# Kernel tuning notes

Hardware: AMD Instinct MI355X
Metric: run time of the kernel (lower is better)

The kernel has to match this reference:

```python
import jax, jax.numpy as jnp
import numpy as np

B, N, D, E, H = 16, 1024, 1024, 4, 16


def setup_inputs() -> dict:
    key = jax.random.key(0)
    k1, k2, k3, k4 = jax.random.split(key, 4)
    return {
        "input_tokens": jax.random.normal(k1, (B, N, D), dtype=jnp.float32),
        "expert_mask": jax.random.randint(k2, (B, N), 0, E, dtype=jnp.int32),
        "qkv_w": jax.random.normal(k3, (3 * D, D), dtype=jnp.float32) * 0.02,
        "proj_w": jax.random.normal(k4, (D, D), dtype=jnp.float32) * 0.02,
        "proj_b": jnp.zeros((D,), dtype=jnp.float32),
    }


def reference(input_tokens, expert_mask, qkv_w, proj_w, proj_b):
    b, n, d = input_tokens.shape
    hd = d // H
    scale = 1.0 / np.sqrt(hd).astype(np.float32)
    # nested expert e uses first d_e = D / 2^(E-1-e) features (expert E-1 = full dim)
    d_tok = d // (2 ** (E - 1 - expert_mask))                     # [B, N]
    feat_mask = (jnp.arange(d)[None, None, :] < d_tok[..., None]).astype(input_tokens.dtype)  # [B, N, D]
    # NestedLinearExpand: slice input features per token (== mask), full 3D output
    x_in = input_tokens * feat_mask
    qkv = jnp.einsum('bnd,fd->bnf', x_in, qkv_w).reshape(b, n, 3, H, hd)
    q, k, v = jnp.moveaxis(qkv, 2, 0)                             # each [B, N, H, hd]
    q = q.transpose(0, 2, 1, 3)                                   # [B, H, N, hd]
    k = k.transpose(0, 2, 1, 3)
    v = v.transpose(0, 2, 1, 3)
    scores = jnp.einsum('bhqd,bhkd->bhqk', q, k) * scale          # [B, H, N, N]
    attn = jax.nn.softmax(scores, axis=-1)
    x = jnp.einsum('bhqk,bhkd->bhqd', attn, v)                    # [B, H, N, hd]
    x = x.transpose(0, 2, 1, 3).reshape(b, n, d)
    # NestedLinearContract: full-dim matmul, only first d_e outputs kept per token
    y = jnp.einsum('bnd,fd->bnf', x, proj_w) + proj_b
    return y * feat_mask
```

## Files before the change

### kernel.cpp

```cpp
#include <hip/hip_runtime.h>
#include <hip/hip_bf16.h>


typedef __bf16 bf16_t;
typedef __bf16 bf16x8 __attribute__((ext_vector_type(8)));
typedef __bf16 bf16x4 __attribute__((ext_vector_type(4)));
typedef float f32x4 __attribute__((ext_vector_type(4)));
typedef float f32x16 __attribute__((ext_vector_type(16)));
typedef int i32x4 __attribute__((ext_vector_type(4)));

typedef __attribute__((address_space(1))) void gvoid;
typedef __attribute__((address_space(3))) void lvoid;

#define MFMA16(a, b, c) __builtin_amdgcn_mfma_f32_16x16x32_bf16((a), (b), (c), 0, 0, 0)
#define MFMA32(a, b, c) __builtin_amdgcn_mfma_f32_32x32x16_bf16((a), (b), (c), 0, 0, 0)
#define GLOAD_LDS16(gsrc, ldst) \
  __builtin_amdgcn_global_load_lds((gvoid*)(gsrc), (lvoid*)(ldst), 16, 0, 0)

#define QSCALE 0.18033688f

__device__ __forceinline__ unsigned cvtpk(float lo, float hi) {
  unsigned r;
  asm("v_cvt_pk_bf16_f32 %0, %1, %2" : "=v"(r) : "v"(lo), "v"(hi));
  return r;
}
__device__ __forceinline__ void pl32swap(unsigned& x, unsigned& y) {
  asm("v_permlane32_swap_b32 %0, %1" : "+v"(x), "+v"(y));
}

__global__ __launch_bounds__(256) void sort_batch(
    const int* __restrict__ em, int* __restrict__ perm, int* __restrict__ ems) {
  __shared__ int cnt[4], base[4], cur[4];
  const int b = blockIdx.x, t = threadIdx.x;
  if (t < 4) cnt[t] = 0;
  __syncthreads();
  int e[4];
#pragma unroll
  for (int i = 0; i < 4; ++i) {
    e[i] = em[b * 1024 + t * 4 + i];
    atomicAdd(&cnt[e[i]], 1);
  }
  __syncthreads();
  if (t == 0) {
    base[0] = 0; base[1] = cnt[0];
    base[2] = cnt[0] + cnt[1]; base[3] = cnt[0] + cnt[1] + cnt[2];
    cur[0] = cur[1] = cur[2] = cur[3] = 0;
  }
  __syncthreads();
#pragma unroll
  for (int i = 0; i < 4; ++i) {
    const int pos = base[e[i]] + atomicAdd(&cur[e[i]], 1);
    perm[b * 1024 + pos] = t * 4 + i;
    ems[b * 1024 + pos] = e[i];
  }
}

__global__ __launch_bounds__(256) void prep_tokens(
    const float* __restrict__ x, const int* __restrict__ perm,
    const int* __restrict__ ems, bf16_t* __restrict__ xq) {
  const int prow = blockIdx.x;
  const int orig = (prow & ~1023) + perm[prow];
  const int dt = 128 << ems[prow];
  const int d = threadIdx.x * 4;
  float4 v = ((const float4*)(x + (size_t)orig * 1024))[threadIdx.x];
  const bool keep = d < dt;
  bf16x4 o;
  o[0] = (bf16_t)(keep ? v.x : 0.f);
  o[1] = (bf16_t)(keep ? v.y : 0.f);
  o[2] = (bf16_t)(keep ? v.z : 0.f);
  o[3] = (bf16_t)(keep ? v.w : 0.f);
  *((bf16x4*)(xq + (size_t)prow * 1024 + d)) = o;
}

__global__ __launch_bounds__(256) void conv_w(
    const float* __restrict__ s, bf16_t* __restrict__ dvec) {
  const int i = blockIdx.x * 256 + threadIdx.x;
  float4 v = ((const float4*)s)[i];
  bf16x4 o;
  o[0] = (bf16_t)v.x; o[1] = (bf16_t)v.y; o[2] = (bf16_t)v.z; o[3] = (bf16_t)v.w;
  ((bf16x4*)dvec)[i] = o;
}

template <int EPI>
__global__ __launch_bounds__(512, 2) void gemm256(
    const bf16_t* __restrict__ A, const bf16_t* __restrict__ Bw, int K,
    const int* __restrict__ perm, const int* __restrict__ ems,
    bf16_t* __restrict__ qo, bf16_t* __restrict__ ko, bf16_t* __restrict__ vto,
    float* __restrict__ yout, const float* __restrict__ bias) {
  __shared__ bf16_t lds[2][32768];
  const int tid = threadIdx.x;
  const int lane = tid & 63, w = tid >> 6;
  const int wm = w >> 2, wn = w & 3;
  const int g = lane >> 4, c16 = lane & 15;

  const int bid = blockIdx.x;
  const int rowbase = (bid & 63) * 256;
  const int colbase = (bid >> 6) * 256;

  const int dtmax = 128 << ems[rowbase + 255];

  if constexpr (EPI == 1) {
    if (colbase >= dtmax) {
      const float4 z = make_float4(0.f, 0.f, 0.f, 0.f);
#pragma unroll
      for (int i = 0; i < 32; ++i) {
        const int idx = i * 512 + tid;
        const int r = idx >> 6, c4 = idx & 63;
        const int orow = ((rowbase + r) & ~1023) + perm[rowbase + r];
        ((float4*)(yout + (size_t)orow * 1024 + colbase))[c4] = z;
      }
      return;
    }
  }

  const int NT = (EPI == 0) ? (dtmax >> 6) : (K >> 6);

  const int trow = tid >> 3;
  const int scol = (((tid & 7) ^ (trow & 7)) << 3);
  const bf16_t* pa = A + (size_t)(rowbase + trow) * K + scol;
  const bf16_t* pb = Bw + (size_t)(colbase + trow) * K + scol;

#define STAGE(j, koff, dst)                                       \
  GLOAD_LDS16(((j) < 4 ? pa + (size_t)((j) * 64) * K              \
                       : pb + (size_t)(((j) - 4) * 64) * K) +     \
                  (koff),                                         \
              (dst) + ((j) * 512 + tid) * 8)

#define LDFRAG(base, R, kk)            \
  (*(const bf16x8*)((base) + (size_t)(R) * 64 + \
                    (((((kk) << 2) + g) ^ (c16 & 7)) << 3)))

  f32x4 acc[8][4] = {};

#pragma unroll
  for (int j = 0; j < 8; ++j) STAGE(j, 0, (bf16_t*)lds[0]);
  asm volatile("s_waitcnt vmcnt(0)" ::: "memory");
  __builtin_amdgcn_s_barrier();

  for (int t = 0; t < NT; ++t) {
    const bf16_t* Lb = lds[t & 1];
    const bf16_t* LbB = Lb + 16384;
    const bool pf = (t + 1) < NT;

    if (pf) {
      bf16_t* Sd = (bf16_t*)lds[(t + 1) & 1];
      const int koff = (t + 1) << 6;
#pragma unroll
      for (int j = 0; j < 8; ++j) STAGE(j, koff, Sd);
    }

    bf16x8 af[4][2], af2[4][2], b0[2][2], b1[2][2];
#pragma unroll
    for (int mi = 0; mi < 4; ++mi)
#pragma unroll
      for (int kk = 0; kk < 2; ++kk)
        af[mi][kk] = LDFRAG(Lb, wm * 128 + mi * 16 + c16, kk);
#pragma unroll
    for (int ni = 0; ni < 2; ++ni)
#pragma unroll
      for (int kk = 0; kk < 2; ++kk)
        b0[ni][kk] = LDFRAG(LbB, wn * 64 + ni * 16 + c16, kk);
#pragma unroll
    for (int mi = 0; mi < 4; ++mi)
#pragma unroll
      for (int ni = 0; ni < 2; ++ni)
#pragma unroll
        for (int kk = 0; kk < 2; ++kk)
          acc[mi][ni] = MFMA16(af[mi][kk], b0[ni][kk], acc[mi][ni]);

#pragma unroll
    for (int ni = 0; ni < 2; ++ni)
#pragma unroll
      for (int kk = 0; kk < 2; ++kk)
        b1[ni][kk] = LDFRAG(LbB, wn * 64 + (ni + 2) * 16 + c16, kk);
#pragma unroll
    for (int mi = 0; mi < 4; ++mi)
#pragma unroll
      for (int ni = 0; ni < 2; ++ni)
#pragma unroll
        for (int kk = 0; kk < 2; ++kk)
          acc[mi][ni + 2] = MFMA16(af[mi][kk], b1[ni][kk], acc[mi][ni + 2]);

#pragma unroll
    for (int mi = 0; mi < 4; ++mi)
#pragma unroll
      for (int kk = 0; kk < 2; ++kk)
        af2[mi][kk] = LDFRAG(Lb, wm * 128 + (mi + 4) * 16 + c16, kk);
#pragma unroll
    for (int mi = 0; mi < 4; ++mi)
#pragma unroll
      for (int ni = 0; ni < 2; ++ni)
#pragma unroll
        for (int kk = 0; kk < 2; ++kk)
          acc[mi + 4][ni] = MFMA16(af2[mi][kk], b0[ni][kk], acc[mi + 4][ni]);

#pragma unroll
    for (int mi = 0; mi < 4; ++mi)
#pragma unroll
      for (int ni = 0; ni < 2; ++ni)
#pragma unroll
        for (int kk = 0; kk < 2; ++kk)
          acc[mi + 4][ni + 2] = MFMA16(af2[mi][kk], b1[ni][kk], acc[mi + 4][ni + 2]);

    if (pf) asm volatile("s_waitcnt vmcnt(0)" ::: "memory");
    __builtin_amdgcn_s_barrier();
  }

  if constexpr (EPI == 0) {
    const int s = colbase >> 10;
#pragma unroll
    for (int mi = 0; mi < 8; ++mi)
#pragma unroll
      for (int j = 0; j < 4; ++j) {
        const int row = rowbase + wm * 128 + mi * 16 + g * 4 + j;
        const int bb = row >> 10, n = row & 1023;
#pragma unroll
        for (int ni = 0; ni < 4; ++ni) {
          const int col = colbase + wn * 64 + ni * 16 + c16;
          const float v = acc[mi][ni][j];
          const int h = (col >> 6) & 15, e = col & 63;
          const size_t bh = (size_t)(bb * 16 + h);
          if (s == 0)
            qo[(bh * 1024 + n) * 64 + e] = (bf16_t)(v * QSCALE);
          else if (s == 1)
            ko[(bh * 1024 + n) * 64 + e] = (bf16_t)v;
          else
            vto[(bh * 64 + e) * 1024 + n] = (bf16_t)v;
        }
      }
  } else {
#pragma unroll
    for (int mi = 0; mi < 8; ++mi)
#pragma unroll
      for (int j = 0; j < 4; ++j) {
        const int row = rowbase + wm * 128 + mi * 16 + g * 4 + j;
        const int dt = 128 << ems[row];
        const int orow = (row & ~1023) + perm[row];
#pragma unroll
        for (int ni = 0; ni < 4; ++ni) {
          const int col = colbase + wn * 64 + ni * 16 + c16;
          const float v = acc[mi][ni][j] + bias[col];
          yout[(size_t)orow * 1024 + col] = (col < dt) ? v : 0.f;
        }
      }
  }
#undef STAGE
#undef LDFRAG
}

__global__ __launch_bounds__(512, 2) void attn256(
    const bf16_t* __restrict__ Q, const bf16_t* __restrict__ Kb,
    const bf16_t* __restrict__ VT, bf16_t* __restrict__ X) {
  __shared__ bf16_t Klds[2][4096];
  __shared__ bf16_t Vlds[2][4096];
  const int tid = threadIdx.x;
  const int w = tid >> 6, lane = tid & 63;
  const int k32 = lane & 31, q5 = lane >> 5;
  const int bh = blockIdx.y;
  const int qbase = blockIdx.x * 256 + w * 32;

  const bf16_t* Qbh = Q + (size_t)bh * 65536;
  const bf16_t* Kbh = Kb + (size_t)bh * 65536;
  const bf16_t* Vbh = VT + (size_t)bh * 65536;

  const int trow = tid >> 3;
  const int tslot = (tid & 7) ^ (trow & 7);
  const bf16_t* kg = Kbh + (size_t)trow * 64 + tslot * 8;
  const bf16_t* vg = Vbh + (size_t)trow * 1024 + tslot * 8;

  bf16x8 qf[4];
#pragma unroll
  for (int kc = 0; kc < 4; ++kc)
    qf[kc] = *(const bf16x8*)(Qbh + (size_t)(qbase + k32) * 64 + kc * 16 + q5 * 8);
  asm volatile("" ::"v"(qf[0]), "v"(qf[1]), "v"(qf[2]), "v"(qf[3]));

  const int rbase = k32 * 128 + q5 * 16;
  const int rswz = (k32 & 7) << 4;

  f32x16 O0 = {}, O1 = {};
  float m = -3.0e38f, lsum = 0.f;

  GLOAD_LDS16(kg, (bf16_t*)Klds[0] + tid * 8);
  GLOAD_LDS16(vg, (bf16_t*)Vlds[0] + tid * 8);

  for (int step = 0; step < 16; ++step) {
    const int buf = step & 1;
    if (step < 15) {
      GLOAD_LDS16(kg + (step + 1) * 4096, (bf16_t*)Klds[buf ^ 1] + tid * 8);
      GLOAD_LDS16(vg + (step + 1) * 64, (bf16_t*)Vlds[buf ^ 1] + tid * 8);
      asm volatile("s_waitcnt vmcnt(2)" ::: "memory");
    } else {
      asm volatile("s_waitcnt vmcnt(0)" ::: "memory");
    }
    __builtin_amdgcn_s_barrier();

    const char* Kl = (const char*)Klds[buf];
    const char* Vl = (const char*)Vlds[buf];

    f32x16 S0 = {}, S1 = {};
#pragma unroll
    for (int kc = 0; kc < 4; ++kc) {
      const int off = (rbase + kc * 32) ^ rswz;
      bf16x8 kf0 = *(const bf16x8*)(Kl + off);
      bf16x8 kf1 = *(const bf16x8*)(Kl + off + 4096);
      S0 = MFMA32(kf0, qf[kc], S0);
      S1 = MFMA32(kf1, qf[kc], S1);
    }

    float pm = fmaxf(S0[0], S1[0]);
#pragma unroll
    for (int r = 1; r < 16; ++r) pm = fmaxf(pm, fmaxf(S0[r], S1[r]));
    pm = fmaxf(pm, __shfl_xor(pm, 32));
    if (__any(pm > m + 8.f)) {
      const float mnew = fmaxf(m, pm);
      const float corr = __builtin_amdgcn_exp2f(m - mnew);
      m = mnew;
      lsum *= corr;
      const int ci = __builtin_bit_cast(int, corr);
#pragma unroll
      for (int r = 0; r < 16; ++r) {
        const int qsel = (r & 3) + 8 * (r >> 2) + 4 * q5;
        const float cr = __builtin_bit_cast(
            float, __builtin_amdgcn_ds_bpermute(qsel << 2, ci));
        O0[r] *= cr;
        O1[r] *= cr;
      }
    }
    float ps = 0.f;
#pragma unroll
    for (int r = 0; r < 16; ++r) {
      float p = __builtin_amdgcn_exp2f(S0[r] - m);
      ps += p; S0[r] = p;
      p = __builtin_amdgcn_exp2f(S1[r] - m);
      ps += p; S1[r] = p;
    }
    lsum += ps;

#define MAKE_PA(PV, B0, PA)                            \
  {                                                    \
    unsigned a_ = cvtpk(PV[B0 + 0], PV[B0 + 1]);       \
    unsigned b_ = cvtpk(PV[B0 + 2], PV[B0 + 3]);       \
    unsigned c_ = cvtpk(PV[B0 + 4], PV[B0 + 5]);       \
    unsigned d_ = cvtpk(PV[B0 + 6], PV[B0 + 7]);       \
    pl32swap(a_, c_);                                  \
    pl32swap(b_, d_);                                  \
    i32x4 wv_;                                         \
    wv_[0] = a_; wv_[1] = b_; wv_[2] = c_; wv_[3] = d_; \
    PA = __builtin_bit_cast(bf16x8, wv_);              \
  }
#define PV_STEP(PV, B0, KS)                                       \
  {                                                               \
    bf16x8 pa;                                                    \
    MAKE_PA(PV, B0, pa);                                          \
    const int voff = (rbase + (KS) * 32) ^ rswz;                  \
    bf16x8 vf0 = *(const bf16x8*)(Vl + voff);                     \
    bf16x8 vf1 = *(const bf16x8*)(Vl + voff + 4096);              \
    O0 = MFMA32(pa, vf0, O0);                                     \
    O1 = MFMA32(pa, vf1, O1);                                     \
  }
    PV_STEP(S0, 0, 0)
    PV_STEP(S0, 8, 1)
    PV_STEP(S1, 0, 2)
    PV_STEP(S1, 8, 3)

    __builtin_amdgcn_s_barrier();
  }

  lsum += __shfl_xor(lsum, 32);
  const float rinv = 1.f / lsum;
  const int ri = __builtin_bit_cast(int, rinv);
  const int bb = bh >> 4, h = bh & 15;
  bf16_t* Xb = X + (size_t)bb * 1024 * 1024 + h * 64;
#pragma unroll
  for (int r = 0; r < 16; ++r) {
    const int qsel = (r & 3) + 8 * (r >> 2) + 4 * q5;
    const float rv = __builtin_bit_cast(
        float, __builtin_amdgcn_ds_bpermute(qsel << 2, ri));
    const size_t rowoff = (size_t)(qbase + qsel) * 1024;
    Xb[rowoff + k32] = (bf16_t)(O0[r] * rv);
    Xb[rowoff + 32 + k32] = (bf16_t)(O1[r] * rv);
  }
}

extern "C" void kernel_launch(void* const* d_in, const int* in_sizes, int n_in,
                              void* d_out, int out_size, void* d_ws,
                              size_t ws_size, hipStream_t stream) {
  const float* x = (const float*)d_in[0];
  const int* em = (const int*)d_in[1];
  const float* qkvw = (const float*)d_in[2];
  const float* projw = (const float*)d_in[3];
  const float* projb = (const float*)d_in[4];
  float* out = (float*)d_out;

  char* ws = (char*)d_ws;
  size_t off = 0;
  bf16_t* xin = (bf16_t*)(ws + off); off += (size_t)16384 * 1024 * 2;
  bf16_t* wq  = (bf16_t*)(ws + off); off += (size_t)3072 * 1024 * 2;
  bf16_t* wp  = (bf16_t*)(ws + off); off += (size_t)1024 * 1024 * 2;
  bf16_t* Qb  = (bf16_t*)(ws + off); off += (size_t)256 * 1024 * 64 * 2;
  bf16_t* Kb  = (bf16_t*)(ws + off); off += (size_t)256 * 1024 * 64 * 2;
  bf16_t* VTb = (bf16_t*)(ws + off); off += (size_t)256 * 64 * 1024 * 2;
  int* perm   = (int*)(ws + off); off += 16384 * 4;
  int* ems    = (int*)(ws + off); off += 16384 * 4;

  sort_batch<<<16, 256, 0, stream>>>(em, perm, ems);

  prep_tokens<<<16384, 256, 0, stream>>>(x, perm, ems, xin);
  conv_w<<<3072, 256, 0, stream>>>(qkvw, wq);
  conv_w<<<1024, 256, 0, stream>>>(projw, wp);

  gemm256<0><<<768, 512, 0, stream>>>(
      xin, wq, 1024, perm, ems, Qb, Kb, VTb, nullptr, nullptr);

  attn256<<<dim3(4, 256), 512, 0, stream>>>(Qb, Kb, VTb, xin);

  gemm256<1><<<256, 512, 0, stream>>>(
      xin, wp, 1024, perm, ems, nullptr, nullptr, nullptr, out, projb);
}
```

Baseline: 295.0 us.

## Interleave GEMM global-to-LDS prefetch with MFMA phases using fine-grained barriers

Restructures the GEMM main loop into an unrolled two-tile, eight-phase schedule. Each phase issues a slice of the next tile's global_load_lds staging between LDS fragment reads and MFMA clusters, replacing the previous bulk prefetch and full vmcnt(0) wait. It adds s_setprio around MFMA blocks, sched_barriers, and partial vmcnt(4) waits so loads overlap compute and the A register footprint drops. The cost is many more workgroup barriers per tile, and correctness depends on NT being even and on the exact order in which staged buffers are reused.

```diff
diff --git a/kernel.cpp b/kernel.cpp
--- a/kernel.cpp
+++ b/kernel.cpp
@@ -130,80 +130,102 @@
   (*(const bf16x8*)((base) + (size_t)(R) * 64 + \
                     (((((kk) << 2) + g) ^ (c16 & 7)) << 3)))
 
+#define LD_A4(F, BASE, ROFF)                                         \
+  _Pragma("unroll") for (int mi = 0; mi < 4; ++mi)                   \
+  _Pragma("unroll") for (int kk = 0; kk < 2; ++kk)                   \
+      F[mi][kk] = LDFRAG((BASE), wm * 128 + ((ROFF) + mi) * 16 + c16, kk);
+#define LD_B2(F, BASE, NOFF)                                         \
+  _Pragma("unroll") for (int ni = 0; ni < 2; ++ni)                   \
+  _Pragma("unroll") for (int kk = 0; kk < 2; ++kk)                   \
+      F[ni][kk] = LDFRAG((BASE), wn * 64 + ((NOFF) + ni) * 16 + c16, kk);
+#define QUAD(MOFF, NOFF, AF, BF)                                     \
+  _Pragma("unroll") for (int mi = 0; mi < 4; ++mi)                   \
+  _Pragma("unroll") for (int ni = 0; ni < 2; ++ni)                   \
+  _Pragma("unroll") for (int kk = 0; kk < 2; ++kk)                   \
+      acc[(MOFF) + mi][(NOFF) + ni] =                                \
+          MFMA16(AF[mi][kk], BF[ni][kk], acc[(MOFF) + mi][(NOFF) + ni]);
+
+#define SB __builtin_amdgcn_sched_barrier(0)
+#define BAR __builtin_amdgcn_s_barrier()
+#define PRIO(x) __builtin_amdgcn_s_setprio(x)
+#define VM4 asm volatile("s_waitcnt vmcnt(4)" ::: "memory")
+#define VM0 asm volatile("s_waitcnt vmcnt(0)" ::: "memory")
+
   f32x4 acc[8][4] = {};
-
-#pragma unroll
-  for (int j = 0; j < 8; ++j) STAGE(j, 0, (bf16_t*)lds[0]);
-  asm volatile("s_waitcnt vmcnt(0)" ::: "memory");
-  __builtin_amdgcn_s_barrier();
-
-  for (int t = 0; t < NT; ++t) {
-    const bf16_t* Lb = lds[t & 1];
-    const bf16_t* LbB = Lb + 16384;
-    const bool pf = (t + 1) < NT;
-
-    if (pf) {
-      bf16_t* Sd = (bf16_t*)lds[(t + 1) & 1];
-      const int koff = (t + 1) << 6;
-#pragma unroll
-      for (int j = 0; j < 8; ++j) STAGE(j, koff, Sd);
-    }
-
-    bf16x8 af[4][2], af2[4][2], b0[2][2], b1[2][2];
-#pragma unroll
-    for (int mi = 0; mi < 4; ++mi)
-#pragma unroll
-      for (int kk = 0; kk < 2; ++kk)
-        af[mi][kk] = LDFRAG(Lb, wm * 128 + mi * 16 + c16, kk);
-#pragma unroll
-    for (int ni = 0; ni < 2; ++ni)
-#pragma unroll
-      for (int kk = 0; kk < 2; ++kk)
-        b0[ni][kk] = LDFRAG(LbB, wn * 64 + ni * 16 + c16, kk);
-#pragma unroll
-    for (int mi = 0; mi < 4; ++mi)
-#pragma unroll
-      for (int ni = 0; ni < 2; ++ni)
-#pragma unroll
-        for (int kk = 0; kk < 2; ++kk)
-          acc[mi][ni] = MFMA16(af[mi][kk], b0[ni][kk], acc[mi][ni]);
-
-#pragma unroll
-    for (int ni = 0; ni < 2; ++ni)
-#pragma unroll
-      for (int kk = 0; kk < 2; ++kk)
-        b1[ni][kk] = LDFRAG(LbB, wn * 64 + (ni + 2) * 16 + c16, kk);
-#pragma unroll
-    for (int mi = 0; mi < 4; ++mi)
-#pragma unroll
-      for (int ni = 0; ni < 2; ++ni)
-#pragma unroll
-        for (int kk = 0; kk < 2; ++kk)
-          acc[mi][ni + 2] = MFMA16(af[mi][kk], b1[ni][kk], acc[mi][ni + 2]);
-
-#pragma unroll
-    for (int mi = 0; mi < 4; ++mi)
-#pragma unroll
-      for (int kk = 0; kk < 2; ++kk)
-        af2[mi][kk] = LDFRAG(Lb, wm * 128 + (mi + 4) * 16 + c16, kk);
-#pragma unroll
-    for (int mi = 0; mi < 4; ++mi)
-#pragma unroll
-      for (int ni = 0; ni < 2; ++ni)
-#pragma unroll
-        for (int kk = 0; kk < 2; ++kk)
-          acc[mi + 4][ni] = MFMA16(af2[mi][kk], b0[ni][kk], acc[mi + 4][ni]);
-
-#pragma unroll
-    for (int mi = 0; mi < 4; ++mi)
-#pragma unroll
-      for (int ni = 0; ni < 2; ++ni)
-#pragma unroll
-        for (int kk = 0; kk < 2; ++kk)
-          acc[mi + 4][ni + 2] = MFMA16(af2[mi][kk], b1[ni][kk], acc[mi + 4][ni + 2]);
-
-    if (pf) asm volatile("s_waitcnt vmcnt(0)" ::: "memory");
-    __builtin_amdgcn_s_barrier();
+  bf16_t* const L0 = (bf16_t*)lds[0];
+  bf16_t* const L1 = (bf16_t*)lds[1];
+  const bf16_t* const L0B = L0 + 16384;
+  const bf16_t* const L1B = L1 + 16384;
+
+#pragma unroll
+  for (int j = 0; j < 8; ++j) STAGE(j, 0, L0);
+  STAGE(0, 64, L1); STAGE(1, 64, L1);
+  STAGE(4, 64, L1); STAGE(5, 64, L1);
+  VM4;
+  BAR; SB;
+
+  for (int t = 0; t < NT; t += 2) {
+    const int k1 = (t + 1) << 6, k2 = (t + 2) << 6, k3 = (t + 3) << 6;
+    const bool pf = (t + 2) < NT;
+    bf16x8 af[4][2], b0[2][2], b1[2][2];
+
+    LD_A4(af, L0, 0);
+    LD_B2(b0, L0B, 0);
+    SB;
+    STAGE(2, k1, L1); STAGE(3, k1, L1);
+    BAR; PRIO(1);
+    QUAD(0, 0, af, b0);
+    PRIO(0); BAR; SB;
+
+    LD_B2(b1, L0B, 2);
+    SB;
+    STAGE(6, k1, L1); STAGE(7, k1, L1);
+    BAR; PRIO(1);
+    QUAD(0, 2, af, b1);
+    PRIO(0); BAR; SB;
+
+    LD_A4(af, L0, 4);
+    SB;
+    if (pf) { STAGE(4, k2, L0); STAGE(5, k2, L0); }
+    BAR; PRIO(1);
+    QUAD(4, 0, af, b0);
+    PRIO(0); BAR; SB;
+
+    if (pf) { STAGE(0, k2, L0); STAGE(1, k2, L0); }
+    PRIO(1);
+    QUAD(4, 2, af, b1);
+    PRIO(0);
+    if (pf) { VM4; } else { VM0; }
+    BAR; SB;
+
+    LD_A4(af, L1, 0);
+    LD_B2(b0, L1B, 0);
+    SB;
+    if (pf) { STAGE(2, k2, L0); STAGE(3, k2, L0); }
+    BAR; PRIO(1);
+    QUAD(0, 0, af, b0);
+    PRIO(0); BAR; SB;
+
+    LD_B2(b1, L1B, 2);
+    SB;
+    if (pf) { STAGE(6, k2, L0); STAGE(7, k2, L0); }
+    BAR; PRIO(1);
+    QUAD(0, 2, af, b1);
+    PRIO(0); BAR; SB;
+
+    LD_A4(af, L1, 4);
+    SB;
+    if (pf) { STAGE(4, k3, L1); STAGE(5, k3, L1); }
+    BAR; PRIO(1);
+    QUAD(4, 0, af, b0);
+    PRIO(0); BAR; SB;
+
+    if (pf) { STAGE(0, k3, L1); STAGE(1, k3, L1); }
+    PRIO(1);
+    QUAD(4, 2, af, b1);
+    PRIO(0);
+    if (pf) { VM4; } else { VM0; }
+    BAR; SB;
   }
 
   if constexpr (EPI == 0) {
@@ -246,6 +268,14 @@
   }
 #undef STAGE
 #undef LDFRAG
+#undef LD_A4
+#undef LD_B2
+#undef QUAD
+#undef SB
+#undef BAR
+#undef PRIO
+#undef VM4
+#undef VM0
 }
 
 __global__ __launch_bounds__(512, 2) void attn256(
```

Result: slower. 303.0 us (+2.7%).
